# Kernel optimization log

Hardware: AMD Instinct MI355X
Metric: run time of the kernel (lower is better)

## Reference

```python
import jax, jax.numpy as jnp
import numpy as np

B, N, DIM = 2, 2048, 1024
H, DH = 16, 64
INNER = H * DH            # 1024
FF_INNER = 4 * DIM        # 4096
EPS = 1e-5


def _layer_norm(x, g, b):
    mu = jnp.mean(x, axis=-1, keepdims=True)
    var = jnp.mean(jnp.square(x - mu), axis=-1, keepdims=True)
    return (x - mu) * jax.lax.rsqrt(var + EPS) * g + b


def _self_attention(x, wq, wk, wv, wo, bo):
    # wq/wk/wv: [INNER, DIM] (torch Linear layout, y = x @ W^T)
    b, n, _ = x.shape
    q = jnp.einsum('bnd,id->bni', x, wq).reshape(b, n, H, DH).transpose(0, 2, 1, 3)
    k = jnp.einsum('bnd,id->bni', x, wk).reshape(b, n, H, DH).transpose(0, 2, 1, 3)
    v = jnp.einsum('bnd,id->bni', x, wv).reshape(b, n, H, DH).transpose(0, 2, 1, 3)
    scale = DH ** -0.5
    sim = jnp.einsum('bhid,bhjd->bhij', q, k) * scale   # [B,H,N,N]
    attn = jax.nn.softmax(sim, axis=-1)
    out = jnp.einsum('bhij,bhjd->bhid', attn, v)
    out = out.transpose(0, 2, 1, 3).reshape(b, n, INNER)
    return jnp.einsum('bni,di->bnd', out, wo) + bo


def _geglu_ff(x, w1, b1, w2, b2):
    # w1: [2*FF_INNER, DIM], w2: [DIM, FF_INNER]
    h = jnp.einsum('bnd,id->bni', x, w1) + b1
    a, gate = jnp.split(h, 2, axis=-1)
    h = a * jax.nn.gelu(gate, approximate=False)
    return jnp.einsum('bni,di->bnd', h, w2) + b2


def setup_inputs() -> dict:
    key = jax.random.key(0)
    ks = jax.random.split(key, 12)
    s = 0.02
    inp = {
        'x': jax.random.normal(ks[0], (B, N, DIM), jnp.float32),
        'ln1_g': jnp.ones((DIM,), jnp.float32),
        'ln1_b': jnp.zeros((DIM,), jnp.float32),
        'w_q1': jax.random.normal(ks[1], (INNER, DIM), jnp.float32) * s,
        'w_k1': jax.random.normal(ks[2], (INNER, DIM), jnp.float32) * s,
        'w_v1': jax.random.normal(ks[3], (INNER, DIM), jnp.float32) * s,
        'w_o1': jax.random.normal(ks[4], (DIM, INNER), jnp.float32) * s,
        'b_o1': jnp.zeros((DIM,), jnp.float32),
        'ln2_g': jnp.ones((DIM,), jnp.float32),
        'ln2_b': jnp.zeros((DIM,), jnp.float32),
        'w_q2': jax.random.normal(ks[5], (INNER, DIM), jnp.float32) * s,
        'w_k2': jax.random.normal(ks[6], (INNER, DIM), jnp.float32) * s,
        'w_v2': jax.random.normal(ks[7], (INNER, DIM), jnp.float32) * s,
        'w_o2': jax.random.normal(ks[8], (DIM, INNER), jnp.float32) * s,
        'b_o2': jnp.zeros((DIM,), jnp.float32),
        'ln3_g': jnp.ones((DIM,), jnp.float32),
        'ln3_b': jnp.zeros((DIM,), jnp.float32),
        'w_ff1': jax.random.normal(ks[9], (2 * FF_INNER, DIM), jnp.float32) * s,
        'b_ff1': jnp.zeros((2 * FF_INNER,), jnp.float32),
        'w_ff2': jax.random.normal(ks[10], (DIM, FF_INNER), jnp.float32) * s,
        'b_ff2': jnp.zeros((DIM,), jnp.float32),
    }
    return inp


def reference(x, ln1_g, ln1_b, w_q1, w_k1, w_v1, w_o1, b_o1,
              ln2_g, ln2_b, w_q2, w_k2, w_v2, w_o2, b_o2,
              ln3_g, ln3_b, w_ff1, b_ff1, w_ff2, b_ff2):
    # attn1 (self) + residual
    x = _self_attention(_layer_norm(x, ln1_g, ln1_b), w_q1, w_k1, w_v1, w_o1, b_o1) + x
    # attn2 (self, context=None) + residual
    x = _self_attention(_layer_norm(x, ln2_g, ln2_b), w_q2, w_k2, w_v2, w_o2, b_o2) + x
    # GEGLU feed-forward + residual
    x = _geglu_ff(_layer_norm(x, ln3_g, ln3_b), w_ff1, b_ff1, w_ff2, b_ff2) + x
    return x
```

## Files before the change

### kernel.cpp

```cpp
#include <hip/hip_runtime.h>
#include <hip/hip_bf16.h>

using bf16x8 = __attribute__((ext_vector_type(8))) short;
using f32x4  = __attribute__((ext_vector_type(4))) float;
using f32x16 = __attribute__((ext_vector_type(16))) float;
typedef unsigned int u32;
typedef unsigned short u16;
using u32x4 = __attribute__((ext_vector_type(4))) u32;

__device__ __forceinline__ u16 f2b(float f) {
  union { float f; u32 u; } v; v.f = f;
  return (u16)((v.u + 0x7FFFu + ((v.u >> 16) & 1u)) >> 16);
}

__device__ __forceinline__ u32 cvtpk(float lo, float hi) {
  u32 r;
  asm("v_cvt_pk_bf16_f32 %0, %1, %2" : "=v"(r) : "v"(lo), "v"(hi));
  return r;
}

__device__ __forceinline__ void gload16(const void* g, void* l) {
  __builtin_amdgcn_global_load_lds((const __attribute__((address_space(1))) u32*)g,
                                   (__attribute__((address_space(3))) u32*)l, 16, 0, 0);
}

__device__ __forceinline__ float gelu_fast(float x) {
  const float x2 = x * x;
  const float t = x * fmaf(0.044715f, x2, 1.f);
  const float u = exp2f(2.3022080f * t);
  return x * u * __builtin_amdgcn_rcpf(u + 1.f);
}

__global__ __launch_bounds__(256) void castall(
    const float* __restrict__ wq1, const float* __restrict__ wk1,
    const float* __restrict__ wv1, const float* __restrict__ wo1,
    const float* __restrict__ wq2, const float* __restrict__ wk2,
    const float* __restrict__ wv2, const float* __restrict__ wo2,
    const float* __restrict__ wff1, const float* __restrict__ wff2,
    u16* __restrict__ qkv1, u16* __restrict__ o1,
    u16* __restrict__ qkv2, u16* __restrict__ o2,
    u16* __restrict__ ff1p, u16* __restrict__ ff2) {
  const long e = ((long)blockIdx.x * 256 + threadIdx.x) * 4;
  constexpr long M1 = 1l << 20;
  const float* s; u16* d;
  if (e < 3 * M1) {
    s = (e < M1 ? wq1 + e : (e < 2 * M1 ? wk1 + (e - M1) : wv1 + (e - 2 * M1)));
    d = qkv1 + e;
  } else if (e < 4 * M1) {
    s = wo1 + (e - 3 * M1); d = o1 + (e - 3 * M1);
  } else if (e < 7 * M1) {
    long r = e - 4 * M1;
    s = (r < M1 ? wq2 + r : (r < 2 * M1 ? wk2 + (r - M1) : wv2 + (r - 2 * M1)));
    d = qkv2 + r;
  } else if (e < 8 * M1) {
    s = wo2 + (e - 7 * M1); d = o2 + (e - 7 * M1);
  } else if (e < 16 * M1) {
    long r = e - 8 * M1;
    long p = r >> 10, col = r & 1023;
    long g = p >> 5, rr = p & 31;
    long lr = (rr < 16) ? (g << 4) + rr : 4096 + (g << 4) + (rr - 16);
    s = wff1 + (lr << 10) + col; d = ff1p + r;
  } else {
    long r = e - 16 * M1;
    s = wff2 + r; d = ff2 + r;
  }
  float4 v = *(const float4*)s;
  ushort4 o;
  o.x = f2b(v.x); o.y = f2b(v.y); o.z = f2b(v.z); o.w = f2b(v.w);
  *(ushort4*)d = o;
}

__global__ __launch_bounds__(256) void ln_kernel(const float* __restrict__ x,
                                                 const float* __restrict__ g,
                                                 const float* __restrict__ b,
                                                 u16* __restrict__ y) {
  const int row = blockIdx.x;
  const int t = threadIdx.x;
  const float* xr = x + (size_t)row * 1024;
  float4 v = ((const float4*)xr)[t];
  float s  = v.x + v.y + v.z + v.w;
  float s2 = v.x * v.x + v.y * v.y + v.z * v.z + v.w * v.w;
  #pragma unroll
  for (int m = 1; m < 64; m <<= 1) {
    s  += __shfl_xor(s, m);
    s2 += __shfl_xor(s2, m);
  }
  __shared__ float red[8];
  if ((t & 63) == 0) { red[(t >> 6) * 2] = s; red[(t >> 6) * 2 + 1] = s2; }
  __syncthreads();
  s  = red[0] + red[2] + red[4] + red[6];
  s2 = red[1] + red[3] + red[5] + red[7];
  const float mu = s * (1.f / 1024.f);
  const float var = s2 * (1.f / 1024.f) - mu * mu;
  const float rs = rsqrtf(var + 1e-5f);
  float4 gv = ((const float4*)g)[t];
  float4 bv = ((const float4*)b)[t];
  ushort4 o;
  o.x = f2b((v.x - mu) * rs * gv.x + bv.x);
  o.y = f2b((v.y - mu) * rs * gv.y + bv.y);
  o.z = f2b((v.z - mu) * rs * gv.z + bv.z);
  o.w = f2b((v.w - mu) * rs * gv.w + bv.w);
  ((ushort4*)(y + (size_t)row * 1024))[t] = o;
}

__global__ __launch_bounds__(512, 4) void gemm_out(
    const u16* __restrict__ A, const u16* __restrict__ Bw,
    const float* __restrict__ bias, const float* __restrict__ resid,
    float* __restrict__ out, int N, int K) {
  extern __shared__ u16 lds[];
  const int tid = threadIdx.x;
  const int l = tid & 63, wid = tid >> 6;
  const int li = l & 15, lg = l >> 4;
  const int wr = wid >> 2, wc = wid & 3;
  const int nx = N >> 7;
  const int cpx = gridDim.x >> 3;
  const int v = (blockIdx.x & 7) * cpx + (blockIdx.x >> 3);
  const int by = v / nx, bx = v - by * nx;
  const int m0 = by << 7, n0 = bx << 7;

  const int sr = tid >> 3;
  const int sc = ((tid & 7) ^ (sr & 7)) << 3;
  const int dc = (tid & 7) << 3;
  const int sc0 = (lg * 8) ^ ((li & 7) << 3);
  const int sc1 = sc0 ^ 32;

  f32x4 acc[4][2] = {};

  auto stageA = [&](int kb, int t2) {
    #pragma unroll
    for (int s = 0; s < 2; ++s)
      gload16(A + (size_t)(m0 + s * 64 + sr) * K + t2 * 64 + sc,
              lds + kb * 8192 + (s * 64 + sr) * 64 + dc);
  };
  auto stageB = [&](int kb, int t2) {
    #pragma unroll
    for (int s = 0; s < 2; ++s)
      gload16(Bw + (size_t)(n0 + s * 64 + sr) * K + t2 * 64 + sc,
              lds + 16384 + kb * 8192 + (s * 64 + sr) * 64 + dc);
  };

  const int NT = K >> 6;
  stageA(0, 0); stageB(0, 0);
  stageA(1, 1); stageB(1, 1);
  asm volatile("s_waitcnt vmcnt(4)" ::: "memory");
  __builtin_amdgcn_s_barrier();

  for (int t = 0; t < NT; ++t) {
    const int kb = t & 1;
    const u16* Ab = lds + kb * 8192 + (wr * 64 + li) * 64;
    const u16* Bb = lds + 16384 + kb * 8192 + (wc * 32 + li) * 64;
    bf16x8 a[4], b[2];

    #pragma unroll
    for (int mi = 0; mi < 4; ++mi) a[mi] = *(const bf16x8*)(Ab + mi * 1024 + sc0);
    #pragma unroll
    for (int n = 0; n < 2; ++n)  b[n]  = *(const bf16x8*)(Bb + n * 1024 + sc0);
    __builtin_amdgcn_s_barrier();
    __builtin_amdgcn_s_setprio(1);
    #pragma unroll
    for (int mi = 0; mi < 4; ++mi)
      #pragma unroll
      for (int n = 0; n < 2; ++n)
        acc[mi][n] = __builtin_amdgcn_mfma_f32_16x16x32_bf16(a[mi], b[n], acc[mi][n], 0, 0, 0);
    __builtin_amdgcn_s_setprio(0);
    __builtin_amdgcn_s_barrier();

    #pragma unroll
    for (int mi = 0; mi < 4; ++mi) a[mi] = *(const bf16x8*)(Ab + mi * 1024 + sc1);
    #pragma unroll
    for (int n = 0; n < 2; ++n)  b[n]  = *(const bf16x8*)(Bb + n * 1024 + sc1);
    __builtin_amdgcn_s_barrier();
    __builtin_amdgcn_s_setprio(1);
    #pragma unroll
    for (int mi = 0; mi < 4; ++mi)
      #pragma unroll
      for (int n = 0; n < 2; ++n)
        acc[mi][n] = __builtin_amdgcn_mfma_f32_16x16x32_bf16(a[mi], b[n], acc[mi][n], 0, 0, 0);
    __builtin_amdgcn_s_setprio(0);
    if (t + 2 < NT) {
      stageA(kb, t + 2); stageB(kb, t + 2);
      asm volatile("s_waitcnt vmcnt(4)" ::: "memory");
    } else if (t + 2 == NT) {
      asm volatile("s_waitcnt vmcnt(0)" ::: "memory");
    }
    __builtin_amdgcn_s_barrier();
  }

  #pragma unroll
  for (int mi = 0; mi < 4; ++mi) {
    const int m = m0 + wr * 64 + mi * 16 + lg * 4;
    #pragma unroll
    for (int n = 0; n < 2; ++n) {
      const int j = n0 + wc * 32 + n * 16 + li;
      const float bj = bias[j];
      #pragma unroll
      for (int rb = 0; rb < 4; ++rb)
        out[(size_t)(m + rb) * N + j] =
            acc[mi][n][rb] + bj + resid[(size_t)(m + rb) * N + j];
    }
  }
}

#define KLOOP_PROLOGUE()                                                      \
  stageA(0, 0); stageB(0, 0); stageA(1, 0); stageB(1, 0);                     \
  stageA(0, 1); stageB(0, 1);                                                 \
  asm volatile("s_waitcnt vmcnt(4)" ::: "memory");                            \
  __builtin_amdgcn_s_barrier();

#define KLOOP_BODY(NT)                                                        \
  bf16x8 b0[4], b1[4];                                                        \
  for (int t = 0; t < NT; ++t) {                                              \
    const int kb = t & 1;                                                     \
    const u16* Abase0 = lds + (kb * 2 + 0) * 8192 + rowA0;                    \
    const u16* Abase1 = lds + (kb * 2 + 1) * 8192 + rowA0;                    \
    const u16* Bbase  = lds + (kb * 2 + bhn) * 8192 + rowB0;                  \
    bf16x8 a[4];                                                              \
    _Pragma("unroll")                                                         \
    for (int j = 0; j < 4; ++j) a[j]  = *(const bf16x8*)(Abase0 + j * 1024 + sc0); \
    _Pragma("unroll")                                                         \
    for (int n = 0; n < 4; ++n) b0[n] = *(const bf16x8*)(Bbase + n * 1024 + sc0); \
    if (t + 1 < NT) stageA(1, t + 1);                                         \
    __builtin_amdgcn_s_barrier();                                             \
    __builtin_amdgcn_s_setprio(1);                                            \
    _Pragma("unroll")                                                         \
    for (int j = 0; j < 4; ++j)                                               \
      _Pragma("unroll")                                                       \
      for (int n = 0; n < 4; ++n)                                             \
        acc[j][n] = __builtin_amdgcn_mfma_f32_16x16x32_bf16(a[j], b0[n], acc[j][n], 0, 0, 0); \
    __builtin_amdgcn_s_setprio(0);                                            \
    __builtin_amdgcn_s_barrier();                                             \
    _Pragma("unroll")                                                         \
    for (int j = 0; j < 4; ++j) a[j]  = *(const bf16x8*)(Abase0 + j * 1024 + sc1); \
    _Pragma("unroll")                                                         \
    for (int n = 0; n < 4; ++n) b1[n] = *(const bf16x8*)(Bbase + n * 1024 + sc1); \
    if (t + 1 < NT) stageB(1, t + 1);                                         \
    __builtin_amdgcn_s_barrier();                                             \
    __builtin_amdgcn_s_setprio(1);                                            \
    _Pragma("unroll")                                                         \
    for (int j = 0; j < 4; ++j)                                               \
      _Pragma("unroll")                                                       \
      for (int n = 0; n < 4; ++n)                                             \
        acc[j][n] = __builtin_amdgcn_mfma_f32_16x16x32_bf16(a[j], b1[n], acc[j][n], 0, 0, 0); \
    __builtin_amdgcn_s_setprio(0);                                            \
    __builtin_amdgcn_s_barrier();                                             \
    _Pragma("unroll")                                                         \
    for (int j = 0; j < 4; ++j) a[j] = *(const bf16x8*)(Abase1 + j * 1024 + sc0); \
    if (t + 2 < NT) stageA(0, t + 2);                                         \
    __builtin_amdgcn_s_barrier();                                             \
    __builtin_amdgcn_s_setprio(1);                                            \
    _Pragma("unroll")                                                         \
    for (int j = 0; j < 4; ++j)                                               \
      _Pragma("unroll")                                                       \
      for (int n = 0; n < 4; ++n)                                             \
        acc[4 + j][n] = __builtin_amdgcn_mfma_f32_16x16x32_bf16(a[j], b0[n], acc[4 + j][n], 0, 0, 0); \
    __builtin_amdgcn_s_setprio(0);                                            \
    __builtin_amdgcn_s_barrier();                                             \
    _Pragma("unroll")                                                         \
    for (int j = 0; j < 4; ++j) a[j] = *(const bf16x8*)(Abase1 + j * 1024 + sc1); \
    if (t + 2 < NT) stageB(0, t + 2);                                         \
    __builtin_amdgcn_s_barrier();                                             \
    __builtin_amdgcn_s_setprio(1);                                            \
    _Pragma("unroll")                                                         \
    for (int j = 0; j < 4; ++j)                                               \
      _Pragma("unroll")                                                       \
      for (int n = 0; n < 4; ++n)                                             \
        acc[4 + j][n] = __builtin_amdgcn_mfma_f32_16x16x32_bf16(a[j], b1[n], acc[4 + j][n], 0, 0, 0); \
    __builtin_amdgcn_s_setprio(0);                                            \
    if (t < NT - 2)       asm volatile("s_waitcnt vmcnt(4)" ::: "memory");    \
    else if (t == NT - 2) asm volatile("s_waitcnt vmcnt(0)" ::: "memory");    \
    __builtin_amdgcn_s_barrier();                                             \
  }

__global__ __launch_bounds__(512, 2) void gemm_ff1(
    const u16* __restrict__ A, const u16* __restrict__ Wp,
    const float* __restrict__ bias, u16* __restrict__ out) {
  extern __shared__ u16 lds[];
  const int tid = threadIdx.x;
  const int l = tid & 63, wid = tid >> 6;
  const int li = l & 15, lg = l >> 4;
  const int wr = wid >> 2, wc = wid & 3;
  const int v = ((blockIdx.x & 7) << 6) + (blockIdx.x >> 3);
  const int bx = v >> 4, by = v & 15;

  const int lr8 = l >> 3;
  const int scb = ((l & 7) ^ lr8) << 3;
  const int sc0 = (lg * 8) ^ ((li & 7) << 3);
  const int sc1 = sc0 ^ 32;

  const int rowA0 = (wr * 64 + li) * 64;
  const int rowB0 = 32768 + ((wc & 1) * 64 + li) * 64;
  const int bhn = wc >> 1;

  f32x4 acc[8][4] = {};

  auto stageA = [&](int h, int t2) {
    const int kb2 = t2 & 1;
    #pragma unroll
    for (int s = 0; s < 2; ++s) {
      const u16* g = A + (size_t)(by * 256 + s * 128 + h * 64 + wid * 8 + lr8) * 1024
                       + t2 * 64 + scb;
      u16* d = lds + (kb2 * 2 + h) * 8192 + s * 4096 + wid * 512;
      gload16(g, d);
    }
  };
  auto stageB = [&](int h, int t2) {
    const int kb2 = t2 & 1;
    #pragma unroll
    for (int s = 0; s < 2; ++s) {
      const u16* g = Wp + (size_t)(bx * 256 + h * 128 + s * 64 + wid * 8 + lr8) * 1024
                        + t2 * 64 + scb;
      u16* d = lds + 32768 + (kb2 * 2 + h) * 8192 + s * 4096 + wid * 512;
      gload16(g, d);
    }
  };

  KLOOP_PROLOGUE()
  KLOOP_BODY(16)

  #pragma unroll
  for (int nj = 0; nj < 2; ++nj) {
    const int c = bx * 128 + wc * 32 + nj * 16 + li;
    const float ba = bias[c];
    const float bg = bias[4096 + c];
    #pragma unroll
    for (int mi = 0; mi < 8; ++mi) {
      #pragma unroll
      for (int rb = 0; rb < 4; ++rb) {
        const float av = acc[mi][2 * nj][rb] + ba;
        const float gv = acc[mi][2 * nj + 1][rb] + bg;
        out[(size_t)(by * 256 + wr * 128 + mi * 16 + lg * 4 + rb) * 4096 + c]
            = f2b(av * gelu_fast(gv));
      }
    }
  }
}

__global__ __launch_bounds__(512, 2) void gemm_qkv(
    const u16* __restrict__ A, const u16* __restrict__ Wp,
    u16* __restrict__ outp) {
  extern __shared__ u16 lds[];
  const int tid = threadIdx.x;
  const int l = tid & 63, wid = tid >> 6;
  const int li = l & 15, lg = l >> 4;
  const int wr = wid >> 2, wc = wid & 3;
  const int v = (blockIdx.x & 7) * 24 + (blockIdx.x >> 3);
  const int bx = v >> 4, by = v & 15;

  const int lr8 = l >> 3;
  const int scb = ((l & 7) ^ lr8) << 3;
  const int sc0 = (lg * 8) ^ ((li & 7) << 3);
  const int sc1 = sc0 ^ 32;

  const int rowA0 = (wr * 64 + li) * 64;
  const int rowB0 = 32768 + ((wc & 1) * 64 + li) * 64;
  const int bhn = wc >> 1;

  f32x4 acc[8][4] = {};

  auto stageA = [&](int h, int t2) {
    const int kb2 = t2 & 1;
    #pragma unroll
    for (int s = 0; s < 2; ++s) {
      const u16* g = A + (size_t)(by * 256 + s * 128 + h * 64 + wid * 8 + lr8) * 1024
                       + t2 * 64 + scb;
      u16* d = lds + (kb2 * 2 + h) * 8192 + s * 4096 + wid * 512;
      gload16(g, d);
    }
  };
  auto stageB = [&](int h, int t2) {
    const int kb2 = t2 & 1;
    #pragma unroll
    for (int s = 0; s < 2; ++s) {
      const u16* g = Wp + (size_t)(bx * 256 + h * 128 + s * 64 + wid * 8 + lr8) * 1024
                        + t2 * 64 + scb;
      u16* d = lds + 32768 + (kb2 * 2 + h) * 8192 + s * 4096 + wid * 512;
      gload16(g, d);
    }
  };

  KLOOP_PROLOGUE()
  KLOOP_BODY(16)

  #pragma unroll
  for (int mi = 0; mi < 8; ++mi) {
    const int mbase = by * 256 + wr * 128 + mi * 16 + lg * 4;
    #pragma unroll
    for (int ni = 0; ni < 4; ++ni) {
      const int j = bx * 256 + wc * 64 + ni * 16 + li;
      f32x4 a = acc[mi][ni];
      const int sec = j >> 10, jj = j & 1023;
      const int h = jj >> 6, dd = jj & 63;
      u16* base = outp + (size_t)sec * 4194304;
      if (sec == 0) {
        #pragma unroll
        for (int rb = 0; rb < 4; ++rb) {
          const int m = mbase + rb;
          const int bb = m >> 11, n = m & 2047;
          base[(((size_t)bb * 16 + h) * 2048 + n) * 64 + dd] =
              f2b(a[rb] * 0.18033688011112042f);
        }
      } else if (sec == 1) {
        #pragma unroll
        for (int rb = 0; rb < 4; ++rb) {
          const int m = mbase + rb;
          const int bb = m >> 11, n = m & 2047;
          base[(((size_t)bb * 16 + h) * 2048 + n) * 64 + (dd ^ ((n & 7) << 3))] =
              f2b(a[rb]);
        }
      } else {
        const int bb = mbase >> 11, n = mbase & 2047;
        const int ng = n & ~63, nl = n & 63;
        const int nl2 = (nl & 51) | ((nl & 4) << 1) | ((nl & 8) >> 1);
        const int col = ng | (nl2 ^ ((dd & 7) << 3));
        ushort4 pk;
        pk.x = f2b(a[0]); pk.y = f2b(a[1]); pk.z = f2b(a[2]); pk.w = f2b(a[3]);
        *(ushort4*)&base[(((size_t)bb * 16 + h) * 64 + dd) * 2048 + col] = pk;
      }
    }
  }
}

__global__ __launch_bounds__(256) void attn_fwd(
    const u16* __restrict__ Q, const u16* __restrict__ K,
    const u16* __restrict__ Vt, u16* __restrict__ Out) {
  __shared__ u16 smem[2][8192];
  const int tid = threadIdx.x;
  const int l = tid & 63, w = tid >> 6;
  const int lo = l & 31, hi = l >> 5, l7 = l & 7;
  const int bh = blockIdx.x & 31, qt = blockIdx.x >> 5;
  const int b_ = bh >> 4, h = bh & 15;

  const u16* Qg = Q + ((size_t)bh * 2048 + qt * 128 + w * 32 + lo) * 64;
  const u16* Kg = K + (size_t)bh * 2048 * 64;
  const u16* Vg = Vt + (size_t)bh * 64 * 2048;

  bf16x8 qf[4];
  #pragma unroll
  for (int d = 0; d < 4; ++d) qf[d] = *(const bf16x8*)&Qg[d * 16 + hi * 8];

  f32x16 o0 = {}, o1 = {};
  float mrow = -1e30f, lrow = 0.f;

  auto stageK = [&](int buf, int jt) {
    #pragma unroll
    for (int i = 0; i < 2; ++i)
      gload16(Kg + (size_t)jt * 4096 + i * 2048 + tid * 8,
              &smem[buf][i * 2048 + w * 512]);
  };
  auto stageV = [&](int buf, int jt) {
    #pragma unroll
    for (int i = 0; i < 2; ++i)
      gload16(Vg + (size_t)(w * 8 + (l >> 3) + i * 32) * 2048 + jt * 64 + l7 * 8,
              &smem[buf][4096 + i * 2048 + w * 512]);
  };

  stageK(0, 0); stageV(0, 0);

  for (int jt = 0; jt < 32; ++jt) {
    const int cur = jt & 1;
    asm volatile("s_waitcnt vmcnt(0)" ::: "memory");
    __builtin_amdgcn_s_barrier();
    if (jt + 1 < 32) { stageK(cur ^ 1, jt + 1); stageV(cur ^ 1, jt + 1); }

    const u16* Kl = &smem[cur][0];
    const u16* Vl = &smem[cur][4096];

    f32x16 st[2] = {};
    #pragma unroll
    for (int dc = 0; dc < 4; ++dc)
      #pragma unroll
      for (int kh = 0; kh < 2; ++kh) {
        const bf16x8 kf = *(const bf16x8*)
            &Kl[(kh * 32 + lo) * 64 + ((dc * 16 + hi * 8) ^ (l7 << 3))];
        st[kh] = __builtin_amdgcn_mfma_f32_32x32x16_bf16(kf, qf[dc], st[kh], 0, 0, 0);
      }

    float pm = st[0][0];
    #pragma unroll
    for (int r = 1; r < 16; ++r) pm = fmaxf(pm, st[0][r]);
    #pragma unroll
    for (int r = 0; r < 16; ++r) pm = fmaxf(pm, st[1][r]);
    pm = fmaxf(pm, __shfl_xor(pm, 32));

    float mn = fmaxf(mrow, pm);
    float fact = 1.f;
    if (__all(mn - mrow <= 8.f)) {
      mn = mrow;
    } else {
      fact = exp2f(mrow - mn);
      mrow = mn;
      #pragma unroll
      for (int r = 0; r < 16; ++r) { o0[r] *= fact; o1[r] *= fact; }
    }

    float p[32];
    float rs = 0.f;
    #pragma unroll
    for (int r = 0; r < 16; ++r) { p[r] = exp2f(st[0][r] - mn); rs += p[r]; }
    #pragma unroll
    for (int r = 0; r < 16; ++r) { p[16 + r] = exp2f(st[1][r] - mn); rs += p[16 + r]; }
    rs += __shfl_xor(rs, 32);
    lrow = lrow * fact + rs;

    bf16x8 pf[4];
    #pragma unroll
    for (int kp = 0; kp < 4; ++kp) {
      u32x4 wv;
      #pragma unroll
      for (int t2 = 0; t2 < 4; ++t2)
        wv[t2] = cvtpk(p[(kp >> 1) * 16 + (kp & 1) * 8 + t2 * 2],
                       p[(kp >> 1) * 16 + (kp & 1) * 8 + t2 * 2 + 1]);
      union { u32x4 a; bf16x8 b; } cc; cc.a = wv;
      pf[kp] = cc.b;
    }

    #pragma unroll
    for (int kp = 0; kp < 4; ++kp) {
      const bf16x8 vf0 = *(const bf16x8*)
          &Vl[lo * 64 + ((kp * 16 + hi * 8) ^ (l7 << 3))];
      o0 = __builtin_amdgcn_mfma_f32_32x32x16_bf16(vf0, pf[kp], o0, 0, 0, 0);
      const bf16x8 vf1 = *(const bf16x8*)
          &Vl[(32 + lo) * 64 + ((kp * 16 + hi * 8) ^ (l7 << 3))];
      o1 = __builtin_amdgcn_mfma_f32_32x32x16_bf16(vf1, pf[kp], o1, 0, 0, 0);
    }
    __builtin_amdgcn_s_barrier();
  }

  const float inv = 1.f / lrow;
  u16* Ob = Out + ((size_t)b_ * 2048 + qt * 128 + w * 32 + lo) * 1024 + h * 64;
  #pragma unroll
  for (int dd = 0; dd < 2; ++dd) {
    #pragma unroll
    for (int R = 0; R < 4; ++R) {
      ushort4 pk;
      const f32x16 oo = dd ? o1 : o0;
      pk.x = f2b(oo[4 * R + 0] * inv); pk.y = f2b(oo[4 * R + 1] * inv);
      pk.z = f2b(oo[4 * R + 2] * inv); pk.w = f2b(oo[4 * R + 3] * inv);
      *(ushort4*)&Ob[dd * 32 + 8 * R + 4 * hi] = pk;
    }
  }
}

extern "C" void kernel_launch(void* const* d_in, const int* in_sizes, int n_in,
                              void* d_out, int out_size, void* d_ws, size_t ws_size,
                              hipStream_t stream) {
  const float* x    = (const float*)d_in[0];
  const float* ln1g = (const float*)d_in[1];
  const float* ln1b = (const float*)d_in[2];
  const float* wq1  = (const float*)d_in[3];
  const float* wk1  = (const float*)d_in[4];
  const float* wv1  = (const float*)d_in[5];
  const float* wo1  = (const float*)d_in[6];
  const float* bo1  = (const float*)d_in[7];
  const float* ln2g = (const float*)d_in[8];
  const float* ln2b = (const float*)d_in[9];
  const float* wq2  = (const float*)d_in[10];
  const float* wk2  = (const float*)d_in[11];
  const float* wv2  = (const float*)d_in[12];
  const float* wo2  = (const float*)d_in[13];
  const float* bo2  = (const float*)d_in[14];
  const float* ln3g = (const float*)d_in[15];
  const float* ln3b = (const float*)d_in[16];
  const float* wff1 = (const float*)d_in[17];
  const float* bff1 = (const float*)d_in[18];
  const float* wff2 = (const float*)d_in[19];
  const float* bff2 = (const float*)d_in[20];

  char* ws = (char*)d_ws;
  const size_t MB = 1024 * 1024;
  u16* wqkv1b = (u16*)(ws + 0 * MB);
  u16* wo1b   = (u16*)(ws + 6 * MB);
  u16* wqkv2b = (u16*)(ws + 8 * MB);
  u16* wo2b   = (u16*)(ws + 14 * MB);
  u16* wff1p  = (u16*)(ws + 16 * MB);
  u16* wff2b  = (u16*)(ws + 32 * MB);
  u16* xn     = (u16*)(ws + 40 * MB);
  u16* Qb     = (u16*)(ws + 48 * MB);
  float* x1   = (float*)(ws + 72 * MB);
  float* x2   = (float*)(ws + 88 * MB);
  u16* hact   = (u16*)(ws + 48 * MB);
  u16* Kb  = Qb + 4194304;
  u16* Vtb = Qb + 8388608;

  hipFuncSetAttribute((const void*)gemm_ff1,
                      hipFuncAttributeMaxDynamicSharedMemorySize, 131072);
  hipFuncSetAttribute((const void*)gemm_qkv,
                      hipFuncAttributeMaxDynamicSharedMemorySize, 131072);
  hipFuncSetAttribute((const void*)gemm_out,
                      hipFuncAttributeMaxDynamicSharedMemorySize, 65536);

  castall<<<20480, 256, 0, stream>>>(wq1, wk1, wv1, wo1, wq2, wk2, wv2, wo2,
                                     wff1, wff2,
                                     wqkv1b, wo1b, wqkv2b, wo2b, wff1p, wff2b);

  ln_kernel<<<4096, 256, 0, stream>>>(x, ln1g, ln1b, xn);
  gemm_qkv<<<192, 512, 131072, stream>>>(xn, wqkv1b, Qb);
  attn_fwd<<<512, 256, 0, stream>>>(Qb, Kb, Vtb, xn);
  gemm_out<<<256, 512, 65536, stream>>>(xn, wo1b, bo1, x, x1, 1024, 1024);

  ln_kernel<<<4096, 256, 0, stream>>>(x1, ln2g, ln2b, xn);
  gemm_qkv<<<192, 512, 131072, stream>>>(xn, wqkv2b, Qb);
  attn_fwd<<<512, 256, 0, stream>>>(Qb, Kb, Vtb, xn);
  gemm_out<<<256, 512, 65536, stream>>>(xn, wo2b, bo2, x1, x2, 1024, 1024);

  ln_kernel<<<4096, 256, 0, stream>>>(x2, ln3g, ln3b, xn);
  gemm_ff1<<<512, 512, 131072, stream>>>(xn, wff1p, bff1, hact);
  gemm_out<<<256, 512, 65536, stream>>>(hact, wff2b, bff2, x2, (float*)d_out, 1024, 4096);
}
```

Measured before the change: 404.0 us.

## Triple-buffer attention K/V staging and hoist LDS fragment loads

The attention kernel moves from double to triple-buffered K/V staging, prefetching two tiles ahead with graded vmcnt waits. The trailing barrier is dropped, and all K and V fragments are loaded from LDS up front. Max and sum reductions become tree-shaped, exp2f is replaced by raw v_exp_f32, and launch bounds request 2 blocks per CU. Sched_barriers are also added to the GEMM prologues. This aims to hide global-load latency and shorten dependency chains, at the cost of more LDS (48KB per block) and registers, which may limit occupancy.

```diff
diff --git a/kernel.cpp b/kernel.cpp
--- a/kernel.cpp
+++ b/kernel.cpp
@@ -16,6 +16,12 @@
 __device__ __forceinline__ u32 cvtpk(float lo, float hi) {
   u32 r;
   asm("v_cvt_pk_bf16_f32 %0, %1, %2" : "=v"(r) : "v"(lo), "v"(hi));
+  return r;
+}
+
+__device__ __forceinline__ float exp2_raw(float x) {
+  float r;
+  asm("v_exp_f32 %0, %1" : "=v"(r) : "v"(x));
   return r;
 }
 
@@ -141,9 +147,12 @@
 
   const int NT = K >> 6;
   stageA(0, 0); stageB(0, 0);
+  __builtin_amdgcn_sched_barrier(0);
   stageA(1, 1); stageB(1, 1);
+  __builtin_amdgcn_sched_barrier(0);
   asm volatile("s_waitcnt vmcnt(4)" ::: "memory");
   __builtin_amdgcn_s_barrier();
+  __builtin_amdgcn_sched_barrier(0);
 
   for (int t = 0; t < NT; ++t) {
     const int kb = t & 1;
@@ -184,6 +193,7 @@
       asm volatile("s_waitcnt vmcnt(0)" ::: "memory");
     }
     __builtin_amdgcn_s_barrier();
+    __builtin_amdgcn_sched_barrier(0);
   }
 
   #pragma unroll
@@ -203,9 +213,12 @@
 
 #define KLOOP_PROLOGUE()                                                      \
   stageA(0, 0); stageB(0, 0); stageA(1, 0); stageB(1, 0);                     \
+  __builtin_amdgcn_sched_barrier(0);                                          \
   stageA(0, 1); stageB(0, 1);                                                 \
+  __builtin_amdgcn_sched_barrier(0);                                          \
   asm volatile("s_waitcnt vmcnt(4)" ::: "memory");                            \
-  __builtin_amdgcn_s_barrier();
+  __builtin_amdgcn_s_barrier();                                               \
+  __builtin_amdgcn_sched_barrier(0);
 
 #define KLOOP_BODY(NT)                                                        \
   bf16x8 b0[4], b1[4];                                                        \
@@ -420,10 +433,10 @@
   }
 }
 
-__global__ __launch_bounds__(256) void attn_fwd(
+__global__ __launch_bounds__(256, 2) void attn_fwd(
     const u16* __restrict__ Q, const u16* __restrict__ K,
     const u16* __restrict__ Vt, u16* __restrict__ Out) {
-  __shared__ u16 smem[2][8192];
+  __shared__ u16 smem[3][8192];
   const int tid = threadIdx.x;
   const int l = tid & 63, w = tid >> 6;
   const int lo = l & 31, hi = l >> 5, l7 = l & 7;
@@ -441,65 +454,85 @@
   f32x16 o0 = {}, o1 = {};
   float mrow = -1e30f, lrow = 0.f;
 
-  auto stageK = [&](int buf, int jt) {
+  auto stage = [&](int buf, int jt) {
     #pragma unroll
     for (int i = 0; i < 2; ++i)
       gload16(Kg + (size_t)jt * 4096 + i * 2048 + tid * 8,
               &smem[buf][i * 2048 + w * 512]);
-  };
-  auto stageV = [&](int buf, int jt) {
     #pragma unroll
     for (int i = 0; i < 2; ++i)
       gload16(Vg + (size_t)(w * 8 + (l >> 3) + i * 32) * 2048 + jt * 64 + l7 * 8,
               &smem[buf][4096 + i * 2048 + w * 512]);
   };
 
-  stageK(0, 0); stageV(0, 0);
-
+  __builtin_amdgcn_sched_barrier(0);
+  stage(0, 0);
+  __builtin_amdgcn_sched_barrier(0);
+  stage(1, 1);
+  __builtin_amdgcn_sched_barrier(0);
+
+  int cur = 0, pre = 2;
   for (int jt = 0; jt < 32; ++jt) {
-    const int cur = jt & 1;
-    asm volatile("s_waitcnt vmcnt(0)" ::: "memory");
+    if (jt == 0)      asm volatile("s_waitcnt vmcnt(8)" ::: "memory");
+    else if (jt < 31) asm volatile("s_waitcnt vmcnt(4)" ::: "memory");
+    else              asm volatile("s_waitcnt vmcnt(0)" ::: "memory");
     __builtin_amdgcn_s_barrier();
-    if (jt + 1 < 32) { stageK(cur ^ 1, jt + 1); stageV(cur ^ 1, jt + 1); }
+    __builtin_amdgcn_sched_barrier(0);
+    if (jt + 2 < 32) stage(pre, jt + 2);
 
     const u16* Kl = &smem[cur][0];
     const u16* Vl = &smem[cur][4096];
 
+    bf16x8 kf[4][2], vf0[4], vf1[4];
+    #pragma unroll
+    for (int dc = 0; dc < 4; ++dc) {
+      const int col = (dc * 16 + hi * 8) ^ (l7 << 3);
+      kf[dc][0] = *(const bf16x8*)&Kl[lo * 64 + col];
+      kf[dc][1] = *(const bf16x8*)&Kl[(32 + lo) * 64 + col];
+      vf0[dc]   = *(const bf16x8*)&Vl[lo * 64 + col];
+      vf1[dc]   = *(const bf16x8*)&Vl[(32 + lo) * 64 + col];
+    }
+
     f32x16 st[2] = {};
     #pragma unroll
-    for (int dc = 0; dc < 4; ++dc)
-      #pragma unroll
-      for (int kh = 0; kh < 2; ++kh) {
-        const bf16x8 kf = *(const bf16x8*)
-            &Kl[(kh * 32 + lo) * 64 + ((dc * 16 + hi * 8) ^ (l7 << 3))];
-        st[kh] = __builtin_amdgcn_mfma_f32_32x32x16_bf16(kf, qf[dc], st[kh], 0, 0, 0);
-      }
-
-    float pm = st[0][0];
-    #pragma unroll
-    for (int r = 1; r < 16; ++r) pm = fmaxf(pm, st[0][r]);
-    #pragma unroll
-    for (int r = 0; r < 16; ++r) pm = fmaxf(pm, st[1][r]);
-    pm = fmaxf(pm, __shfl_xor(pm, 32));
+    for (int dc = 0; dc < 4; ++dc) {
+      st[0] = __builtin_amdgcn_mfma_f32_32x32x16_bf16(kf[dc][0], qf[dc], st[0], 0, 0, 0);
+      st[1] = __builtin_amdgcn_mfma_f32_32x32x16_bf16(kf[dc][1], qf[dc], st[1], 0, 0, 0);
+    }
+
+    float mx[8];
+    #pragma unroll
+    for (int r = 0; r < 8; ++r)
+      mx[r] = fmaxf(fmaxf(st[0][r], st[0][r + 8]), fmaxf(st[1][r], st[1][r + 8]));
+    #pragma unroll
+    for (int s2 = 4; s2 >= 1; s2 >>= 1)
+      #pragma unroll
+      for (int r = 0; r < s2; ++r) mx[r] = fmaxf(mx[r], mx[r + s2]);
+    const float pm = fmaxf(mx[0], __shfl_xor(mx[0], 32));
 
     float mn = fmaxf(mrow, pm);
     float fact = 1.f;
     if (__all(mn - mrow <= 8.f)) {
       mn = mrow;
     } else {
-      fact = exp2f(mrow - mn);
+      fact = exp2_raw(mrow - mn);
       mrow = mn;
       #pragma unroll
       for (int r = 0; r < 16; ++r) { o0[r] *= fact; o1[r] *= fact; }
     }
 
-    float p[32];
-    float rs = 0.f;
-    #pragma unroll
-    for (int r = 0; r < 16; ++r) { p[r] = exp2f(st[0][r] - mn); rs += p[r]; }
-    #pragma unroll
-    for (int r = 0; r < 16; ++r) { p[16 + r] = exp2f(st[1][r] - mn); rs += p[16 + r]; }
-    rs += __shfl_xor(rs, 32);
+    float p[32], sm[16];
+    #pragma unroll
+    for (int r = 0; r < 16; ++r) p[r]      = exp2_raw(st[0][r] - mn);
+    #pragma unroll
+    for (int r = 0; r < 16; ++r) p[16 + r] = exp2_raw(st[1][r] - mn);
+    #pragma unroll
+    for (int r = 0; r < 16; ++r) sm[r] = p[r] + p[16 + r];
+    #pragma unroll
+    for (int s2 = 8; s2 >= 1; s2 >>= 1)
+      #pragma unroll
+      for (int r = 0; r < s2; ++r) sm[r] += sm[r + s2];
+    const float rs = sm[0] + __shfl_xor(sm[0], 32);
     lrow = lrow * fact + rs;
 
     bf16x8 pf[4];
@@ -516,14 +549,12 @@
 
     #pragma unroll
     for (int kp = 0; kp < 4; ++kp) {
-      const bf16x8 vf0 = *(const bf16x8*)
-          &Vl[lo * 64 + ((kp * 16 + hi * 8) ^ (l7 << 3))];
-      o0 = __builtin_amdgcn_mfma_f32_32x32x16_bf16(vf0, pf[kp], o0, 0, 0, 0);
-      const bf16x8 vf1 = *(const bf16x8*)
-          &Vl[(32 + lo) * 64 + ((kp * 16 + hi * 8) ^ (l7 << 3))];
-      o1 = __builtin_amdgcn_mfma_f32_32x32x16_bf16(vf1, pf[kp], o1, 0, 0, 0);
-    }
-    __builtin_amdgcn_s_barrier();
+      o0 = __builtin_amdgcn_mfma_f32_32x32x16_bf16(vf0[kp], pf[kp], o0, 0, 0, 0);
+      o1 = __builtin_amdgcn_mfma_f32_32x32x16_bf16(vf1[kp], pf[kp], o1, 0, 0, 0);
+    }
+
+    cur = (cur == 2) ? 0 : cur + 1;
+    pre = (pre == 2) ? 0 : pre + 1;
   }
 
   const float inv = 1.f / lrow;
```

Result: faster. 372.4 us (-7.8%).
